# Optimization experiments

Measured on AMD Instinct MI355X. Metric: run time of the kernel, lower is better.

## Reference

```python
import jax, jax.numpy as jnp
import numpy as np

B, N, C, H = 8, 4096, 768, 8
EPS = 1e-12  # F.normalize eps


def setup_inputs() -> dict:
    key = jax.random.key(0)
    k1, k2, k3, k4 = jax.random.split(key, 4)
    x = jax.random.normal(k1, (B, N, C), dtype=jnp.float32)
    Wqkv = jax.random.normal(k2, (C, 3 * C), dtype=jnp.float32) * (1.0 / np.sqrt(C))
    temperature = jnp.ones((H, 1, 1), dtype=jnp.float32)
    Wproj = jax.random.normal(k3, (C, C), dtype=jnp.float32) * (1.0 / np.sqrt(C))
    bproj = jax.random.normal(k4, (C,), dtype=jnp.float32) * 0.01
    return {"x": x, "Wqkv": Wqkv, "temperature": temperature, "Wproj": Wproj, "bproj": bproj}


def _l2norm(t):
    # F.normalize(dim=-1): t / max(||t||_2, eps)
    n = jnp.sqrt(jnp.sum(t * t, axis=-1, keepdims=True))
    return t / jnp.maximum(n, EPS)


def reference(x, Wqkv, temperature, Wproj, bproj):
    b, n, c = x.shape
    h = temperature.shape[0]
    hd = c // h
    qkv = x @ Wqkv  # [B, N, 3C]
    qkv = qkv.reshape(b, n, 3, h, hd).transpose(2, 0, 3, 4, 1)  # [3, B, H, hd, N]
    q, k, v = qkv[0], qkv[1], qkv[2]
    q = _l2norm(q)  # normalize over token dim N
    k = _l2norm(k)
    # channel-channel attention: [B, H, hd, hd]
    attn = jnp.einsum('bhdn,bhen->bhde', q, k) * temperature  # temperature [H,1,1] broadcasts
    attn = jax.nn.softmax(attn, axis=-1)
    out = jnp.einsum('bhde,bhen->bhdn', attn, v)  # [B, H, hd, N]
    out = out.transpose(0, 3, 1, 2).reshape(b, n, c)  # [B, N, C]
    return out @ Wproj + bproj
```

## Files before the change

### kernel.cpp

```cpp
#include <hip/hip_runtime.h>
#include <stdint.h>


typedef __attribute__((ext_vector_type(8))) __bf16 bf16x8;
typedef __attribute__((ext_vector_type(4))) float f32x4;

__device__ __forceinline__ unsigned short f2b(float f) {
  uint32_t u = __float_as_uint(f);
  u += 0x7FFF + ((u >> 16) & 1);
  return (unsigned short)(u >> 16);
}

__device__ __forceinline__ void gload16(const void* g, void* l) {
  __builtin_amdgcn_global_load_lds(
      (__attribute__((address_space(1))) void*)(uintptr_t)g,
      (__attribute__((address_space(3))) void*)(uintptr_t)l, 16, 0, 0);
}

__global__ void cvt_bf16(const float* __restrict__ in, unsigned short* __restrict__ out, int n4,
                         float* __restrict__ Z, int nz4) {
  int gid = blockIdx.x * blockDim.x + threadIdx.x;
  if (gid < nz4) reinterpret_cast<float4*>(Z)[gid] = make_float4(0.f, 0.f, 0.f, 0.f);
  int stride = gridDim.x * blockDim.x;
  for (int i = gid; i < n4; i += stride) {
    float4 v = reinterpret_cast<const float4*>(in)[i];
    ushort4 o;
    o.x = f2b(v.x); o.y = f2b(v.y); o.z = f2b(v.z); o.w = f2b(v.w);
    reinterpret_cast<ushort4*>(out)[i] = o;
  }
}

__global__ void cvt_transpose(const float* __restrict__ in, unsigned short* __restrict__ out,
                              int K, int NC) {
  __shared__ float tile[32][33];
  int bx = blockIdx.x, by = blockIdx.y;
  int tx = threadIdx.x & 31, ty = threadIdx.x >> 5;
  for (int r = ty; r < 32; r += 8)
    tile[r][tx] = in[(size_t)(by * 32 + r) * NC + bx * 32 + tx];
  __syncthreads();
  for (int r = ty; r < 32; r += 8)
    out[(size_t)(bx * 32 + r) * K + by * 32 + tx] = f2b(tile[tx][r]);
}


#define BARX() asm volatile("s_barrier" ::: "memory")
#define WAITV(N) asm volatile("s_waitcnt vmcnt(" #N ")" ::: "memory")
#define SCHED() __builtin_amdgcn_sched_barrier(0)

#define STAGE(gbase, p, isB, h, t) do {                                             \
  unsigned short* _lb = &lds[(p)*32768 + (isB)*16384 + (h)*8192 + wid*1024];        \
  const unsigned short* _gb = (gbase) + (size_t)((h)*128 + wid*16)*768 + (t)*64 + lanegoff; \
  gload16(_gb, _lb);                                                                \
  gload16(_gb + 8*768, _lb + 512);                                                  \
} while (0)

#define LOAD_AF(p, mh) do {                                                         \
  const unsigned short* _ab = &lds[(p)*32768 + (mh)*8192];                          \
  _Pragma("unroll") for (int _mi = 0; _mi < 4; _mi++)                               \
    _Pragma("unroll") for (int _kk = 0; _kk < 2; _kk++)                             \
      af[_mi][_kk] = *(const bf16x8*)&_ab[(wm*64 + _mi*16 + l16)*64 + ((_kk*4+quad)^(l16&7))*8]; \
} while (0)

#define LOAD_BF(dst, p, nh) do {                                                    \
  const unsigned short* _bb = &lds[(p)*32768 + 16384 + (nh)*8192];                  \
  _Pragma("unroll") for (int _ni = 0; _ni < 2; _ni++)                               \
    _Pragma("unroll") for (int _kk = 0; _kk < 2; _kk++)                             \
      dst[_ni][_kk] = *(const bf16x8*)&_bb[(wn*32 + _ni*16 + l16)*64 + ((_kk*4+quad)^(l16&7))*8]; \
} while (0)

#define MFMA_PH(mh, nh, bfx) do {                                                   \
  __builtin_amdgcn_s_setprio(1);                                                    \
  _Pragma("unroll") for (int _m = 0; _m < 4; _m++)                                  \
    _Pragma("unroll") for (int _n = 0; _n < 2; _n++)                                \
      _Pragma("unroll") for (int _k = 0; _k < 2; _k++)                              \
        acc[(mh)*4+_m][(nh)*2+_n] = __builtin_amdgcn_mfma_f32_16x16x32_bf16(        \
            af[_m][_k], bfx[_n][_k], acc[(mh)*4+_m][(nh)*2+_n], 0, 0, 0);           \
  __builtin_amdgcn_s_setprio(0);                                                    \
} while (0)

__global__ __launch_bounds__(512, 2) void gemm_qkv(
    const unsigned short* __restrict__ A, const unsigned short* __restrict__ Bt,
    unsigned short* __restrict__ qkT, unsigned short* __restrict__ vT,
    float* __restrict__ normsq) {
  __shared__ __align__(16) unsigned short lds[65536];
  int lin = blockIdx.y * 9 + blockIdx.x;
  int swz = (lin & 7) * 144 + (lin >> 3);
  int bm = swz / 9;
  int bj = swz - bm * 9;
  int m0 = bm * 256, j0 = bj * 256;
  int tid = threadIdx.x;
  int wid = tid >> 6, lane = tid & 63;
  int wm = wid >> 2, wn = wid & 3;
  int quad = lane >> 4, l16 = lane & 15;
  int srow = lane >> 3, sch = lane & 7;
  int cmem = sch ^ srow;
  int lanegoff = srow * 768 + cmem * 8;

  f32x4 acc[8][4];
  f32x4 z = {0.f, 0.f, 0.f, 0.f};
#pragma unroll
  for (int i = 0; i < 8; i++)
#pragma unroll
    for (int j = 0; j < 4; j++) acc[i][j] = z;

  bf16x8 af[4][2], bf0[2][2], bf1[2][2];

  const unsigned short* Ab2 = A + (size_t)m0 * 768;
  const unsigned short* Bb2 = Bt + (size_t)j0 * 768;

  STAGE(Ab2, 0, 0, 0, 0); STAGE(Bb2, 0, 1, 0, 0); STAGE(Bb2, 0, 1, 1, 0); STAGE(Ab2, 0, 0, 1, 0);
  STAGE(Ab2, 1, 0, 0, 1); STAGE(Bb2, 1, 1, 0, 1); STAGE(Bb2, 1, 1, 1, 1); STAGE(Ab2, 1, 0, 1, 1);
  WAITV(12);
  BARX();

  for (int t = 0; t < 10; t++) {
    int p = t & 1;
    LOAD_AF(p, 0); LOAD_BF(bf0, p, 0);
    if (t >= 1) STAGE(Ab2, p ^ 1, 0, 1, t + 1);
    BARX(); SCHED();
    MFMA_PH(0, 0, bf0);
    SCHED(); WAITV(10); BARX();
    LOAD_BF(bf1, p, 1);
    STAGE(Ab2, p, 0, 0, t + 2);
    BARX(); SCHED();
    MFMA_PH(0, 1, bf1);
    SCHED(); WAITV(10); BARX();
    LOAD_AF(p, 1);
    STAGE(Bb2, p, 1, 0, t + 2);
    BARX(); SCHED();
    MFMA_PH(1, 1, bf1);
    SCHED(); BARX();
    STAGE(Bb2, p, 1, 1, t + 2);
    BARX(); SCHED();
    MFMA_PH(1, 0, bf0);
    SCHED(); WAITV(10); BARX();
  }
  LOAD_AF(0, 0); LOAD_BF(bf0, 0, 0);
  STAGE(Ab2, 1, 0, 1, 11);
  BARX(); SCHED(); MFMA_PH(0, 0, bf0); SCHED(); WAITV(10); BARX();
  LOAD_BF(bf1, 0, 1);
  BARX(); SCHED(); MFMA_PH(0, 1, bf1); SCHED(); WAITV(8); BARX();
  LOAD_AF(0, 1);
  BARX(); SCHED(); MFMA_PH(1, 1, bf1); SCHED(); BARX();
  BARX(); SCHED(); MFMA_PH(1, 0, bf0); SCHED(); WAITV(4); BARX();
  LOAD_AF(1, 0); LOAD_BF(bf0, 1, 0);
  BARX(); SCHED(); MFMA_PH(0, 0, bf0); SCHED(); WAITV(2); BARX();
  LOAD_BF(bf1, 1, 1);
  BARX(); SCHED(); MFMA_PH(0, 1, bf1); SCHED(); WAITV(0); BARX();
  LOAD_AF(1, 1);
  BARX(); SCHED(); MFMA_PH(1, 1, bf1); SCHED(); BARX();
  BARX(); SCHED(); MFMA_PH(1, 0, bf0); SCHED(); BARX();

  int s = bj / 3;
  int b = m0 >> 12;
  int n0 = m0 & 4095;

  if (s < 2) {
#pragma unroll
    for (int ni = 0; ni < 4; ni++) {
      float ss = 0.f;
#pragma unroll
      for (int mi = 0; mi < 8; mi++)
#pragma unroll
        for (int r = 0; r < 4; r++) ss += acc[mi][ni][r] * acc[mi][ni][r];
      ss += __shfl_down(ss, 32, 64);
      ss += __shfl_down(ss, 16, 64);
      if (lane < 16) {
        int cc = (ni >> 1) * 128 + wn * 32 + (ni & 1) * 16 + l16;
        int local = j0 + cc - s * 768;
        int hh = local / 96, d = local - hh * 96;
        atomicAdd(&normsq[s * 6144 + (b * 8 + hh) * 96 + d], ss);
      }
    }
#pragma unroll
    for (int jh = 0; jh < 2; jh++) {
      __syncthreads();
#pragma unroll
      for (int nl = 0; nl < 2; nl++) {
        int ni = jh * 2 + nl;
        int jc = wn * 32 + nl * 16 + l16;
#pragma unroll
        for (int mi = 0; mi < 8; mi++) {
          int mrow = (mi >> 2) * 128 + wm * 64 + (mi & 3) * 16 + quad * 4;
#pragma unroll
          for (int r = 0; r < 4; r++) lds[jc * 264 + mrow + r] = f2b(acc[mi][ni][r]);
        }
      }
      __syncthreads();
#pragma unroll
      for (int it = 0; it < 8; it++) {
        int id = it * 512 + tid;
        int jr = id >> 5, mc = id & 31;
        int j = j0 + jh * 128 + jr;
        int local = j - s * 768;
        int hh = local / 96, d = local - hh * 96;
        size_t off = ((size_t)(s * 64 + b * 8 + hh) * 96 + d) * 4096 + n0 + mc * 8;
        *(uint4*)&qkT[off] = *(const uint4*)&lds[jr * 264 + mc * 8];
      }
    }
  } else {
    int j0v = j0 - 1536;
#pragma unroll
    for (int mh = 0; mh < 2; mh++) {
      __syncthreads();
#pragma unroll
      for (int ml = 0; ml < 4; ml++) {
        int mi = mh * 4 + ml;
        int mloc = wm * 64 + ml * 16 + quad * 4;
#pragma unroll
        for (int ni = 0; ni < 4; ni++) {
          int jc = (ni >> 1) * 128 + wn * 32 + (ni & 1) * 16 + l16;
#pragma unroll
          for (int r = 0; r < 4; r++) lds[(mloc + r) * 264 + jc] = f2b(acc[mi][ni][r]);
        }
      }
      __syncthreads();
#pragma unroll
      for (int it = 0; it < 8; it++) {
        int id = it * 512 + tid;
        int mr = id >> 5, ch = id & 31;
        int cp = j0v + ch * 8;
        int hh = cp / 96, e = cp - hh * 96;
        size_t off = ((size_t)(b * 8 + hh) * 4096 + (n0 + mh * 128 + mr)) * 96 + e;
        *(uint4*)&vT[off] = *(const uint4*)&lds[mr * 264 + ch * 8];
      }
    }
  }
}

__global__ __launch_bounds__(256, 2) void attn_s(const unsigned short* __restrict__ qkT,
                                                 float* __restrict__ S) {
  __shared__ __align__(16) unsigned short lds[12288];
  int blk = blockIdx.x;
  int bh = blk >> 3, ks = blk & 7;
  const unsigned short* qb = qkT + (size_t)bh * 96 * 4096;
  const unsigned short* kb = qkT + (size_t)(64 + bh) * 96 * 4096;
  int tid = threadIdx.x, wid = tid >> 6, lane = tid & 63;
  int wm = wid >> 1, wn = wid & 1, quad = lane >> 4, l16 = lane & 15;
  int srow = lane >> 3, sch = lane & 7;
  int cmem = sch ^ srow;
  f32x4 acc[3][3];
  f32x4 z = {0.f, 0.f, 0.f, 0.f};
#pragma unroll
  for (int i = 0; i < 3; i++)
#pragma unroll
    for (int j = 0; j < 3; j++) acc[i][j] = z;

  for (int k0 = ks * 512; k0 < ks * 512 + 512; k0 += 64) {
#pragma unroll
    for (int i = 0; i < 3; i++) {
      int ig = wid * 3 + i;
      int row = ig * 8 + srow;
      gload16(qb + (size_t)row * 4096 + k0 + cmem * 8, &lds[ig * 512]);
      gload16(kb + (size_t)row * 4096 + k0 + cmem * 8, &lds[6144 + ig * 512]);
    }
    __syncthreads();
#pragma unroll
    for (int kk = 0; kk < 2; kk++) {
      int cs = ((kk * 4 + quad) ^ (l16 & 7)) * 8;
      bf16x8 af[3], bfr[3];
#pragma unroll
      for (int mi = 0; mi < 3; mi++)
        af[mi] = *(const bf16x8*)&lds[(wm * 48 + mi * 16 + l16) * 64 + cs];
#pragma unroll
      for (int ni = 0; ni < 3; ni++)
        bfr[ni] = *(const bf16x8*)&lds[6144 + (wn * 48 + ni * 16 + l16) * 64 + cs];
#pragma unroll
      for (int mi = 0; mi < 3; mi++)
#pragma unroll
        for (int ni = 0; ni < 3; ni++)
          acc[mi][ni] = __builtin_amdgcn_mfma_f32_16x16x32_bf16(af[mi], bfr[ni], acc[mi][ni], 0, 0, 0);
    }
    __syncthreads();
  }
  float* Sb = S + (size_t)bh * 9216;
#pragma unroll
  for (int mi = 0; mi < 3; mi++)
#pragma unroll
    for (int ni = 0; ni < 3; ni++)
#pragma unroll
      for (int r = 0; r < 4; r++)
        atomicAdd(&Sb[(wm * 48 + mi * 16 + quad * 4 + r) * 96 + wn * 48 + ni * 16 + l16],
                  acc[mi][ni][r]);
}

__global__ __launch_bounds__(128) void softmax96(
    const float* __restrict__ S, const float* __restrict__ normsq,
    const float* __restrict__ temp, unsigned short* __restrict__ attnB) {
  __shared__ float ik[96];
  int bh = blockIdx.x;
  int h = bh & 7;
  int tid = threadIdx.x;
  if (tid < 96) ik[tid] = 1.0f / fmaxf(sqrtf(normsq[6144 + bh * 96 + tid]), 1e-12f);
  __syncthreads();
  if (tid < 96) {
    int d = tid;
    const float* Srow = S + (size_t)bh * 9216 + d * 96;
    float iq = (1.0f / fmaxf(sqrtf(normsq[bh * 96 + d]), 1e-12f)) * temp[h];
    float mx = -1e30f;
    for (int e = 0; e < 96; e++) mx = fmaxf(mx, Srow[e] * iq * ik[e]);
    float sum = 0.f;
    for (int e = 0; e < 96; e++) sum += __expf(Srow[e] * iq * ik[e] - mx);
    float inv = 1.0f / sum;
    unsigned short* row = attnB + (size_t)bh * 9984 + d * 104;
    for (int e = 0; e < 96; e++) row[e] = f2b(__expf(Srow[e] * iq * ik[e] - mx) * inv);
    for (int e = 96; e < 104; e++) row[e] = 0;
  }
}

__global__ __launch_bounds__(256, 2) void attn_v(
    const unsigned short* __restrict__ attnB, const unsigned short* __restrict__ vT,
    unsigned short* __restrict__ U) {
  __shared__ __align__(16) unsigned short lds[23552];
  int blk = blockIdx.x;
  int bh = blk >> 5, nc = blk & 31;
  int b = bh >> 3, h = bh & 7;
  int n0 = nc * 128;
  int tid = threadIdx.x, wid = tid >> 6, lane = tid & 63;
  int wm = wid >> 1, wn = wid & 1, quad = lane >> 4, l16 = lane & 15;

  const unsigned short* ab = attnB + (size_t)bh * 9984;
#pragma unroll
  for (int i = 0; i < 5; i++) {
    int id = i * 256 + tid;
    int ids = id < 1248 ? id : 1247;
    gload16(ab + (size_t)ids * 8, &lds[(i * 4 + wid) * 512]);
  }

  const unsigned short* vb = vT + (size_t)bh * 4096 * 96 + (size_t)n0 * 96;
#pragma unroll
  for (int i = 0; i < 7; i++) {
    int ig = wid + i * 4;
    if (ig < 26) {
      int id = ig * 64 + lane;
      int row = id / 13;
      int ch = id - row * 13;
      if (ch > 11) ch = 11;
      gload16(vb + (size_t)row * 96 + ch * 8, &lds[10240 + ig * 512]);
    }
  }
  __syncthreads();

  f32x4 acc[3][4];
  f32x4 z = {0.f, 0.f, 0.f, 0.f};
#pragma unroll
  for (int i = 0; i < 3; i++)
#pragma unroll
    for (int j = 0; j < 4; j++) acc[i][j] = z;
#pragma unroll
  for (int et = 0; et < 3; et++) {
    bf16x8 af[3], bfr[4];
#pragma unroll
    for (int mi = 0; mi < 3; mi++)
      af[mi] = *(const bf16x8*)&lds[(wm * 48 + mi * 16 + l16) * 104 + (et * 4 + quad) * 8];
#pragma unroll
    for (int ni = 0; ni < 4; ni++)
      bfr[ni] = *(const bf16x8*)&lds[10240 + (wn * 64 + ni * 16 + l16) * 104 + (et * 4 + quad) * 8];
#pragma unroll
    for (int mi = 0; mi < 3; mi++)
#pragma unroll
      for (int ni = 0; ni < 4; ni++)
        acc[mi][ni] = __builtin_amdgcn_mfma_f32_16x16x32_bf16(af[mi], bfr[ni], acc[mi][ni], 0, 0, 0);
  }
  __syncthreads();

#pragma unroll
  for (int mi = 0; mi < 3; mi++)
#pragma unroll
    for (int ni = 0; ni < 4; ni++)
#pragma unroll
      for (int r = 0; r < 4; r++) {
        int d = wm * 48 + mi * 16 + quad * 4 + r;
        int n = wn * 64 + ni * 16 + l16;
        lds[n * 104 + d] = f2b(acc[mi][ni][r]);
      }
  __syncthreads();
#pragma unroll
  for (int it = 0; it < 6; it++) {
    int id = tid + it * 256;
    int nr = id / 12, ch = id - nr * 12;
    *(uint4*)&U[((size_t)(b * 4096 + n0 + nr)) * 768 + h * 96 + ch * 8] =
        *(const uint4*)&lds[nr * 104 + ch * 8];
  }
}

__global__ __launch_bounds__(256, 2) void gemm_out(
    const unsigned short* __restrict__ A, const unsigned short* __restrict__ Bt,
    const float* __restrict__ bias, float* __restrict__ out) {
  __shared__ __align__(16) unsigned short lds[16384];
  int bj = blockIdx.x;
  int bm = blockIdx.y;
  int m0 = bm * 128, j0 = bj * 128;
  int tid = threadIdx.x;
  int wid = tid >> 6, lane = tid & 63;
  int wm = wid >> 1, wn = wid & 1;
  int quad = lane >> 4, l16 = lane & 15;
  int srow = lane >> 3, sch = lane & 7;
  int cmem = sch ^ srow;

  f32x4 acc[4][4];
  f32x4 z = {0.f, 0.f, 0.f, 0.f};
#pragma unroll
  for (int i = 0; i < 4; i++)
#pragma unroll
    for (int j = 0; j < 4; j++) acc[i][j] = z;

  const unsigned short* Ab = A + (size_t)m0 * 768;
  const unsigned short* Bb = Bt + (size_t)j0 * 768;

  for (int k0 = 0; k0 < 768; k0 += 64) {
#pragma unroll
    for (int i = 0; i < 4; i++) {
      int ig = wid * 4 + i;
      int row = ig * 8 + srow;
      gload16(Ab + (size_t)row * 768 + k0 + cmem * 8, &lds[ig * 512]);
      gload16(Bb + (size_t)row * 768 + k0 + cmem * 8, &lds[8192 + ig * 512]);
    }
    __syncthreads();
#pragma unroll
    for (int kk = 0; kk < 2; kk++) {
      int cs = ((kk * 4 + quad) ^ (l16 & 7)) * 8;
      bf16x8 af[4], bfr[4];
#pragma unroll
      for (int mi = 0; mi < 4; mi++)
        af[mi] = *(const bf16x8*)&lds[(wm * 64 + mi * 16 + l16) * 64 + cs];
#pragma unroll
      for (int ni = 0; ni < 4; ni++)
        bfr[ni] = *(const bf16x8*)&lds[8192 + (wn * 64 + ni * 16 + l16) * 64 + cs];
#pragma unroll
      for (int mi = 0; mi < 4; mi++)
#pragma unroll
        for (int ni = 0; ni < 4; ni++)
          acc[mi][ni] = __builtin_amdgcn_mfma_f32_16x16x32_bf16(af[mi], bfr[ni], acc[mi][ni], 0, 0, 0);
    }
    __syncthreads();
  }
#pragma unroll
  for (int ni = 0; ni < 4; ni++) {
    int ccol = j0 + wn * 64 + ni * 16 + l16;
    float bv = bias[ccol];
#pragma unroll
    for (int mi = 0; mi < 4; mi++)
#pragma unroll
      for (int r = 0; r < 4; r++)
        out[(size_t)(m0 + wm * 64 + mi * 16 + quad * 4 + r) * 768 + ccol] = acc[mi][ni][r] + bv;
  }
}

extern "C" void kernel_launch(void* const* d_in, const int* in_sizes, int n_in,
                              void* d_out, int out_size, void* d_ws, size_t ws_size,
                              hipStream_t stream) {
  const float* x = (const float*)d_in[0];
  const float* Wqkv = (const float*)d_in[1];
  const float* temp = (const float*)d_in[2];
  const float* Wproj = (const float*)d_in[3];
  const float* bproj = (const float*)d_in[4];
  float* out = (float*)d_out;
  char* ws = (char*)d_ws;

  unsigned short* xb     = (unsigned short*)(ws);
  unsigned short* WqkvT  = (unsigned short*)(ws + 50331648);
  unsigned short* WprojT = (unsigned short*)(ws + 53870592);
  unsigned short* qkT    = (unsigned short*)(ws + 55050240);
  unsigned short* vT     = (unsigned short*)(ws + 155713536);
  unsigned short* U      = (unsigned short*)(ws + 206045184);
  float* S               = (float*)(ws + 256376832);
  float* normsq          = (float*)(ws + 258736128);
  unsigned short* attnB  = qkT;

  cvt_bf16<<<dim3(4096), dim3(256), 0, stream>>>(x, xb, 25165824 / 4, S, 150528);
  cvt_transpose<<<dim3(72, 24), dim3(256), 0, stream>>>(Wqkv, WqkvT, 768, 2304);
  cvt_transpose<<<dim3(24, 24), dim3(256), 0, stream>>>(Wproj, WprojT, 768, 768);
  gemm_qkv<<<dim3(9, 128), dim3(512), 0, stream>>>(xb, WqkvT, qkT, vT, normsq);
  attn_s<<<dim3(512), dim3(256), 0, stream>>>(qkT, S);
  softmax96<<<dim3(64), dim3(128), 0, stream>>>(S, normsq, temp, attnB);
  attn_v<<<dim3(2048), dim3(256), 0, stream>>>(attnB, vT, U);
  gemm_out<<<dim3(6, 256), dim3(256), 0, stream>>>(U, WprojT, bproj, out);
}
```

Measured before the change: 442.6 us.

## Software-pipeline LDS fragment loads across MFMA phases in QKV GEMM

```diff
diff --git a/kernel.cpp b/kernel.cpp
--- a/kernel.cpp
+++ b/kernel.cpp
@@ -54,14 +54,14 @@
   gload16(_gb + 8*768, _lb + 512);                                                  \
 } while (0)
 
-#define LOAD_AF(p, mh) do {                                                         \
+#define LOAD_A(p, mh) do {                                                          \
   const unsigned short* _ab = &lds[(p)*32768 + (mh)*8192];                          \
   _Pragma("unroll") for (int _mi = 0; _mi < 4; _mi++)                               \
     _Pragma("unroll") for (int _kk = 0; _kk < 2; _kk++)                             \
       af[_mi][_kk] = *(const bf16x8*)&_ab[(wm*64 + _mi*16 + l16)*64 + ((_kk*4+quad)^(l16&7))*8]; \
 } while (0)
 
-#define LOAD_BF(dst, p, nh) do {                                                    \
+#define LOAD_B(dst, p, nh) do {                                                     \
   const unsigned short* _bb = &lds[(p)*32768 + 16384 + (nh)*8192];                  \
   _Pragma("unroll") for (int _ni = 0; _ni < 2; _ni++)                               \
     _Pragma("unroll") for (int _kk = 0; _kk < 2; _kk++)                             \
@@ -109,45 +109,48 @@
   const unsigned short* Bb2 = Bt + (size_t)j0 * 768;
 
   STAGE(Ab2, 0, 0, 0, 0); STAGE(Bb2, 0, 1, 0, 0); STAGE(Bb2, 0, 1, 1, 0); STAGE(Ab2, 0, 0, 1, 0);
-  STAGE(Ab2, 1, 0, 0, 1); STAGE(Bb2, 1, 1, 0, 1); STAGE(Bb2, 1, 1, 1, 1); STAGE(Ab2, 1, 0, 1, 1);
-  WAITV(12);
+  STAGE(Ab2, 1, 0, 0, 1); STAGE(Bb2, 1, 1, 0, 1); STAGE(Bb2, 1, 1, 1, 1);
+  WAITV(10);
+  BARX();
+  LOAD_A(0, 0);
+  LOAD_B(bf0, 0, 0);
+  WAITV(8);
   BARX();
 
   for (int t = 0; t < 10; t++) {
     int p = t & 1;
-    LOAD_AF(p, 0); LOAD_BF(bf0, p, 0);
-    if (t >= 1) STAGE(Ab2, p ^ 1, 0, 1, t + 1);
+    LOAD_B(bf1, p, 1);
+    STAGE(Ab2, p ^ 1, 0, 1, t + 1);
     BARX(); SCHED();
     MFMA_PH(0, 0, bf0);
-    SCHED(); WAITV(10); BARX();
-    LOAD_BF(bf1, p, 1);
+    SCHED(); WAITV(8); BARX();
     STAGE(Ab2, p, 0, 0, t + 2);
     BARX(); SCHED();
     MFMA_PH(0, 1, bf1);
-    SCHED(); WAITV(10); BARX();
-    LOAD_AF(p, 1);
+    SCHED();
+    LOAD_A(p, 1);
+    BARX();
     STAGE(Bb2, p, 1, 0, t + 2);
     BARX(); SCHED();
     MFMA_PH(1, 1, bf1);
-    SCHED(); BARX();
+    SCHED(); WAITV(8); BARX();
     STAGE(Bb2, p, 1, 1, t + 2);
     BARX(); SCHED();
     MFMA_PH(1, 0, bf0);
-    SCHED(); WAITV(10); BARX();
-  }
-  LOAD_AF(0, 0); LOAD_BF(bf0, 0, 0);
+    SCHED();
+    LOAD_A(p ^ 1, 0);
+    LOAD_B(bf0, p ^ 1, 0);
+    WAITV(8); BARX();
+  }
+  LOAD_B(bf1, 0, 1);
   STAGE(Ab2, 1, 0, 1, 11);
-  BARX(); SCHED(); MFMA_PH(0, 0, bf0); SCHED(); WAITV(10); BARX();
-  LOAD_BF(bf1, 0, 1);
-  BARX(); SCHED(); MFMA_PH(0, 1, bf1); SCHED(); WAITV(8); BARX();
-  LOAD_AF(0, 1);
-  BARX(); SCHED(); MFMA_PH(1, 1, bf1); SCHED(); BARX();
-  BARX(); SCHED(); MFMA_PH(1, 0, bf0); SCHED(); WAITV(4); BARX();
-  LOAD_AF(1, 0); LOAD_BF(bf0, 1, 0);
-  BARX(); SCHED(); MFMA_PH(0, 0, bf0); SCHED(); WAITV(2); BARX();
-  LOAD_BF(bf1, 1, 1);
-  BARX(); SCHED(); MFMA_PH(0, 1, bf1); SCHED(); WAITV(0); BARX();
-  LOAD_AF(1, 1);
+  BARX(); SCHED(); MFMA_PH(0, 0, bf0); SCHED(); WAITV(8); BARX();
+  BARX(); SCHED(); MFMA_PH(0, 1, bf1); SCHED(); LOAD_A(0, 1); BARX();
+  BARX(); SCHED(); MFMA_PH(1, 1, bf1); SCHED(); WAITV(4); BARX();
+  BARX(); SCHED(); MFMA_PH(1, 0, bf0); SCHED(); LOAD_A(1, 0); LOAD_B(bf0, 1, 0); WAITV(2); BARX();
+  LOAD_B(bf1, 1, 1);
+  BARX(); SCHED(); MFMA_PH(0, 0, bf0); SCHED(); WAITV(0); BARX();
+  BARX(); SCHED(); MFMA_PH(0, 1, bf1); SCHED(); LOAD_A(1, 1); BARX();
   BARX(); SCHED(); MFMA_PH(1, 1, bf1); SCHED(); BARX();
   BARX(); SCHED(); MFMA_PH(1, 0, bf0); SCHED(); BARX();
 
@@ -308,7 +311,7 @@
   }
 }
 
-__global__ __launch_bounds__(256, 2) void attn_v(
+__global__ __launch_bounds__(256, 4) void attn_v(
     const unsigned short* __restrict__ attnB, const unsigned short* __restrict__ vT,
     unsigned short* __restrict__ U) {
   __shared__ __align__(16) unsigned short lds[23552];
```

Measured after the change: 434.4 us. About the same (-1.8%).
